# Optimization experiments

Hardware: AMD Instinct MI355X
Metric: run time of the kernel (lower is better)

The kernel has to match this reference:

```python
import jax, jax.numpy as jnp
import numpy as np

H_DIM = 1024
NUM_HEADS = 16
HEAD_DIM = H_DIM // NUM_HEADS
EPS = 1e-5


def rms_norm(x, w, eps=EPS):
    var = jnp.mean(jnp.square(x), axis=-1, keepdims=True)
    return x * jax.lax.rsqrt(var + eps) * w


def setup_inputs() -> dict:
    key = jax.random.key(0)
    ks = jax.random.split(key, 8)
    B, S = 2, 2048
    x = jax.random.normal(ks[0], (B, S, H_DIM), dtype=jnp.float32)
    # learned params (orthogonal init approximated by scaled normal for a correctness baseline)
    qkv_w = jax.random.normal(ks[1], (3 * H_DIM, H_DIM), dtype=jnp.float32) / np.sqrt(H_DIM)
    gate_w = jax.random.normal(ks[2], (NUM_HEADS, H_DIM), dtype=jnp.float32) / np.sqrt(H_DIM)
    o_w = jax.random.normal(ks[3], (H_DIM, H_DIM), dtype=jnp.float32) / np.sqrt(H_DIM)
    prenorm_w = jnp.ones((H_DIM,), dtype=jnp.float32)
    q_norm_w = jnp.ones((HEAD_DIM,), dtype=jnp.float32)
    k_norm_w = jnp.ones((HEAD_DIM,), dtype=jnp.float32)
    return {"x": x, "prenorm_w": prenorm_w, "qkv_w": qkv_w, "gate_w": gate_w,
            "o_w": o_w, "q_norm_w": q_norm_w, "k_norm_w": k_norm_w}


def reference(x, prenorm_w, qkv_w, gate_w, o_w, q_norm_w, k_norm_w):
    B, S, D = x.shape
    residual = x
    xn = rms_norm(x, prenorm_w)                                   # [B,S,D]
    qkv = jnp.einsum('bsd,ed->bse', xn, qkv_w)                    # [B,S,3D]
    qkv = qkv.reshape(B, S, 3, NUM_HEADS, HEAD_DIM)
    gate = jnp.einsum('bsd,hd->bsh', xn, gate_w)                  # [B,S,H]
    q, k, v = qkv[:, :, 0], qkv[:, :, 1], qkv[:, :, 2]            # [B,S,H,hd]
    q = rms_norm(q, q_norm_w)
    k = rms_norm(k, k_norm_w)
    scale = 1.0 / np.sqrt(HEAD_DIM).astype(np.float32)
    scores = jnp.einsum('bqhd,bkhd->bhqk', q, k) * scale          # [B,H,S,S]
    attn = jax.nn.softmax(scores, axis=-1)
    out = jnp.einsum('bhqk,bkhd->bhqd', attn, v)                  # [B,H,S,hd]
    out = out * jax.nn.sigmoid(gate).transpose(0, 2, 1)[..., None]
    out = out.transpose(0, 2, 1, 3).reshape(B, S, D)              # [B,S,D]
    return jnp.einsum('bsd,ed->bse', out, o_w) + residual
```

## Files before the change

kernel.cpp:

```cpp
#include <hip/hip_runtime.h>
#include <math.h>

typedef __bf16 bf16x8 __attribute__((ext_vector_type(8)));
typedef float f32x4 __attribute__((ext_vector_type(4)));
typedef float f32x16 __attribute__((ext_vector_type(16)));
typedef unsigned int uint2v __attribute__((ext_vector_type(2)));
typedef unsigned int uint4v __attribute__((ext_vector_type(4)));
typedef unsigned short ushort_t;

#define SEQ 2048
#define MROWS 4096
#define EPS 1e-5f
#define QKS 3200
#define LOG2E 1.4426950408889634f
#define SMAX_B2 17.32f

__device__ __forceinline__ float bf2f(ushort_t u) {
  union { unsigned int i; float f; } c; c.i = ((unsigned int)u) << 16; return c.f;
}
__device__ __forceinline__ ushort_t f2bf(float f) {
  union { unsigned int i; float f; } c; c.f = f;
  unsigned int i = c.i;
  unsigned int r = i + 0x7fffu + ((i >> 16) & 1u);
  return (ushort_t)(r >> 16);
}
__device__ __forceinline__ ushort_t f2bf_fast(float f) {
  union { __bf16 b; ushort_t u; } cv; cv.b = (__bf16)f; return cv.u;
}

__device__ __forceinline__ float exp2_raw(float x) {
  float r; asm("v_exp_f32 %0, %1" : "=v"(r) : "v"(x)); return r;
}

#define CVTPK(d, a, b) asm("v_cvt_pk_bf16_f32 %0, %1, %2" : "=v"(d) : "v"(a), "v"(b))

__device__ __forceinline__ void plane_swap(unsigned int &a, unsigned int &b) {
#if __has_builtin(__builtin_amdgcn_permlane32_swap)
  uint2v r = __builtin_amdgcn_permlane32_swap(a, b, 0, 0);
  a = r.x; b = r.y;
#else
  unsigned int sa = (unsigned int)__shfl_xor((int)a, 32);
  unsigned int sb = (unsigned int)__shfl_xor((int)b, 32);
  int hi = (int)((threadIdx.x & 63) >> 5);
  unsigned int na = hi ? sb : a;
  unsigned int nb = hi ? b : sa;
  a = na; b = nb;
#endif
}

__device__ __forceinline__ void softmax_pack(const f32x16 &stv, float &lp,
                                             uint4v &Fa, uint4v &Fb) {
  float p[16];
  #pragma unroll
  for (int r = 0; r < 16; ++r) p[r] = exp2_raw(stv[r] - SMAX_B2);
  float s0 = (p[0] + p[1]) + (p[2] + p[3]);
  float s1 = (p[4] + p[5]) + (p[6] + p[7]);
  float s2 = (p[8] + p[9]) + (p[10] + p[11]);
  float s3 = (p[12] + p[13]) + (p[14] + p[15]);
  lp += (s0 + s1) + (s2 + s3);
  unsigned int X00, X01, X10, X11, X20, X21, X30, X31;
  CVTPK(X00, p[0], p[1]);   CVTPK(X01, p[2], p[3]);
  CVTPK(X10, p[4], p[5]);   CVTPK(X11, p[6], p[7]);
  CVTPK(X20, p[8], p[9]);   CVTPK(X21, p[10], p[11]);
  CVTPK(X30, p[12], p[13]); CVTPK(X31, p[14], p[15]);
  plane_swap(X00, X10); plane_swap(X01, X11);
  plane_swap(X20, X30); plane_swap(X21, X31);
  Fa.x = X00; Fa.y = X01; Fa.z = X10; Fa.w = X11;
  Fb.x = X20; Fb.y = X21; Fb.z = X30; Fb.w = X31;
}

__device__ __forceinline__ float wave_sum(float v) {
  #pragma unroll
  for (int off = 32; off > 0; off >>= 1) v += __shfl_xor(v, off);
  return v;
}

__global__ void detect_kernel(const unsigned int* __restrict__ xraw, int* __restrict__ flag) {
  int tid = threadIdx.x;
  int cnt = 0;
  for (int i = tid; i < 4096; i += 256) {
    unsigned int e = (xraw[i] >> 7) & 0xFFu;
    cnt += (e >= 100u && e <= 150u) ? 1 : 0;
  }
  __shared__ int sred[256];
  sred[tid] = cnt;
  __syncthreads();
  for (int s = 128; s > 0; s >>= 1) {
    if (tid < s) sred[tid] += sred[tid + s];
    __syncthreads();
  }
  if (tid == 0) flag[0] = (sred[0] > 2048) ? 1 : 0;
}

__global__ void prep_norm_kernel(const void* __restrict__ qkvw_in, const void* __restrict__ gw_in,
                                 const void* __restrict__ ow_in, const void* __restrict__ pw_in,
                                 const void* __restrict__ qn_in, const void* __restrict__ kn_in,
                                 const void* __restrict__ xraw,
                                 ushort_t* __restrict__ Wcat, ushort_t* __restrict__ ow,
                                 float* __restrict__ qnf, float* __restrict__ knf,
                                 ushort_t* __restrict__ xn,
                                 const int* __restrict__ flag) {
  __shared__ float red[4];
  int bid = blockIdx.x, tid = threadIdx.x;
  int bf = *flag;
  if (bid < 3072) {
    long long i4 = (long long)bid * 256 + tid;
    if (bf) {
      ((ushort4*)Wcat)[i4] = ((const ushort4*)qkvw_in)[i4];
    } else {
      float4 f = ((const float4*)qkvw_in)[i4];
      ushort4 o;
      o.x = f2bf(f.x); o.y = f2bf(f.y); o.z = f2bf(f.z); o.w = f2bf(f.w);
      ((ushort4*)Wcat)[i4] = o;
    }
  } else if (bid < 3088) {
    long long j4 = (long long)(bid - 3072) * 256 + tid;
    ushort4* dst = (ushort4*)(Wcat + 3072 * 1024);
    if (bf) {
      dst[j4] = ((const ushort4*)gw_in)[j4];
    } else {
      float4 f = ((const float4*)gw_in)[j4];
      ushort4 o;
      o.x = f2bf(f.x); o.y = f2bf(f.y); o.z = f2bf(f.z); o.w = f2bf(f.w);
      dst[j4] = o;
    }
  } else if (bid < 4112) {
    long long j4 = (long long)(bid - 3088) * 256 + tid;
    if (bf) {
      ((ushort4*)ow)[j4] = ((const ushort4*)ow_in)[j4];
    } else {
      float4 f = ((const float4*)ow_in)[j4];
      ushort4 o;
      o.x = f2bf(f.x); o.y = f2bf(f.y); o.z = f2bf(f.z); o.w = f2bf(f.w);
      ((ushort4*)ow)[j4] = o;
    }
  } else if (bid == 4112) {
    if (tid < 64) {
      qnf[tid] = bf ? bf2f(((const ushort_t*)qn_in)[tid]) : ((const float*)qn_in)[tid];
      knf[tid] = bf ? bf2f(((const ushort_t*)kn_in)[tid]) : ((const float*)kn_in)[tid];
    }
  } else {
    int row = bid - 4113;
    float4 u;
    if (bf) {
      ushort4 s = ((const ushort4*)xraw)[row * 256 + tid];
      u.x = bf2f(s.x); u.y = bf2f(s.y); u.z = bf2f(s.z); u.w = bf2f(s.w);
    } else {
      u = ((const float4*)xraw)[row * 256 + tid];
    }
    float ss = u.x*u.x + u.y*u.y + u.z*u.z + u.w*u.w;
    ss = wave_sum(ss);
    if ((tid & 63) == 0) red[tid >> 6] = ss;
    __syncthreads();
    float total = red[0] + red[1] + red[2] + red[3];
    float inv = rsqrtf(total * (1.0f / 1024.0f) + EPS);
    float4 wu;
    if (bf) {
      ushort4 s = ((const ushort4*)pw_in)[tid];
      wu.x = bf2f(s.x); wu.y = bf2f(s.y); wu.z = bf2f(s.z); wu.w = bf2f(s.w);
    } else {
      wu = ((const float4*)pw_in)[tid];
    }
    ushort4 o;
    o.x = f2bf(u.x * inv * wu.x);
    o.y = f2bf(u.y * inv * wu.y);
    o.z = f2bf(u.z * inv * wu.z);
    o.w = f2bf(u.w * inv * wu.w);
    ((ushort4*)(xn + (long long)row * 1024))[tid] = o;
  }
}

__device__ __forceinline__ void gll16(const ushort_t* g, ushort_t* l) {
  __builtin_amdgcn_global_load_lds(
      (const __attribute__((address_space(1))) unsigned int*)g,
      (__attribute__((address_space(3))) unsigned int*)l, 16, 0, 0);
}

__global__ void gemm_qkv_fused(const ushort_t* __restrict__ A, const ushort_t* __restrict__ B,
                               ushort_t* __restrict__ C, float* __restrict__ gate,
                               ushort_t* __restrict__ Vt,
                               const float* __restrict__ qw, const float* __restrict__ kw) {
  __shared__ char gsm[128 * 136 * 2] __attribute__((aligned(16)));
  ushort_t* As = (ushort_t*)gsm;
  ushort_t* Bs = (ushort_t*)(gsm + 16384);
  int tid = threadIdx.x, wave = tid >> 6, lane = tid & 63;
  int lin = blockIdx.x;
  int xcd = lin & 7;
  int i2 = lin >> 3;
  int my = (xcd << 2) + i2 / 25;
  int nx = i2 % 25;
  int m_blk = my * 128, n_blk = nx * 128;
  int wm = (wave & 1) * 64, wn = (wave >> 1) * 64;
  int g = lane >> 4, c = lane & 15;
  int arow = lane >> 2;
  int akc = (lane & 3) << 3;
  f32x4 acc[4][4] = {};
  for (int kt = 0; kt < 1024; kt += 64) {
    #pragma unroll
    for (int hh = 0; hh < 2; ++hh)
      #pragma unroll
      for (int i = 0; i < 2; ++i) {
        int rbase = (i * 4 + wave) * 16;
        gll16(A + (long long)(m_blk + rbase + arow) * 1024 + kt + hh * 32 + akc,
              &As[hh * 4096 + rbase * 32]);
        gll16(B + (long long)(n_blk + rbase + arow) * 1024 + kt + hh * 32 + akc,
              &Bs[hh * 4096 + rbase * 32]);
      }
    __syncthreads();
    #pragma unroll
    for (int hh = 0; hh < 2; ++hh) {
      bf16x8 af[4], bfr[4];
      #pragma unroll
      for (int mi = 0; mi < 4; ++mi)
        af[mi] = *(const bf16x8*)&As[hh * 4096 + (wm + mi * 16 + c) * 32 + (g << 3)];
      #pragma unroll
      for (int ni = 0; ni < 4; ++ni)
        bfr[ni] = *(const bf16x8*)&Bs[hh * 4096 + (wn + ni * 16 + c) * 32 + (g << 3)];
      #pragma unroll
      for (int mi = 0; mi < 4; ++mi)
        #pragma unroll
        for (int ni = 0; ni < 4; ++ni)
          acc[mi][ni] = __builtin_amdgcn_mfma_f32_16x16x32_bf16(af[mi], bfr[ni], acc[mi][ni], 0, 0, 0);
    }
    __syncthreads();
  }
  int col_base = n_blk + wn;
  if (col_base < 2048) {
    int isk = col_base >= 1024;
    float scale = isk ? 1.0f : (0.125f * LOG2E);
    const float* nw = isk ? kw : qw;
    float w[4];
    #pragma unroll
    for (int ni = 0; ni < 4; ++ni) w[ni] = nw[ni * 16 + c];
    #pragma unroll
    for (int mi = 0; mi < 4; ++mi)
      #pragma unroll
      for (int r = 0; r < 4; ++r) {
        float ss = 0.f;
        #pragma unroll
        for (int ni = 0; ni < 4; ++ni) ss += acc[mi][ni][r] * acc[mi][ni][r];
        #pragma unroll
        for (int off = 8; off > 0; off >>= 1) ss += __shfl_xor(ss, off);
        float inv = rsqrtf(ss * (1.0f / 64.0f) + EPS) * scale;
        int row = m_blk + wm + mi * 16 + g * 4 + r;
        #pragma unroll
        for (int ni = 0; ni < 4; ++ni)
          C[(long long)row * QKS + col_base + ni * 16 + c] = f2bf(acc[mi][ni][r] * inv * w[ni]);
      }
  } else if (n_blk < 3072) {
    ushort_t* vts = (ushort_t*)gsm;
    const int VSTR = 136;
    #pragma unroll
    for (int mi = 0; mi < 4; ++mi)
      #pragma unroll
      for (int r = 0; r < 4; ++r) {
        int row_l = wm + mi * 16 + g * 4 + r;
        #pragma unroll
        for (int ni = 0; ni < 4; ++ni) {
          int col_l = wn + ni * 16 + c;
          vts[col_l * VSTR + row_l] = f2bf(acc[mi][ni][r]);
        }
      }
    __syncthreads();
    int rowv = tid >> 1, half = tid & 1;
    int vcol = (n_blk - 2048) + rowv;
    int h = vcol >> 6, d = vcol & 63;
    int b2 = m_blk >> 11;
    ushort_t* dst = Vt + ((long long)(b2 * 16 + h) * 64 + d) * SEQ + (m_blk & 2047) + half * 64;
    const ushort_t* srcl = &vts[rowv * VSTR + half * 64];
    #pragma unroll
    for (int j = 0; j < 8; ++j)
      *(bf16x8*)(dst + j * 8) = *(const bf16x8*)(srcl + j * 8);
  } else if (col_base == 3072) {
    #pragma unroll
    for (int mi = 0; mi < 4; ++mi)
      #pragma unroll
      for (int r = 0; r < 4; ++r) {
        int row = m_blk + wm + mi * 16 + g * 4 + r;
        float v = acc[mi][0][r];
        gate[(long long)row * 16 + c] = 1.0f / (1.0f + __expf(-v));
      }
  }
}

__global__ void gemm_tiled(const ushort_t* __restrict__ A, const ushort_t* __restrict__ B,
                           void* __restrict__ Cv, const void* __restrict__ res,
                           const int* __restrict__ flag,
                           int K, int lda, int ldb, int ldc) {
  __shared__ ushort_t As[2 * 128 * 32];
  __shared__ ushort_t Bs[2 * 128 * 32];
  int tid = threadIdx.x, wave = tid >> 6, lane = tid & 63;
  int lin = blockIdx.x;
  int xcd = lin & 7;
  int i2 = lin >> 3;
  int my = (xcd << 2) + (i2 >> 3);
  int nx = i2 & 7;
  int m_blk = my * 128, n_blk = nx * 128;
  int wm = (wave & 1) * 64, wn = (wave >> 1) * 64;
  int g = lane >> 4, c = lane & 15;
  int arow = lane >> 2;
  int akc = (lane & 3) << 3;
  f32x4 acc[4][4] = {};
  for (int kt = 0; kt < K; kt += 64) {
    #pragma unroll
    for (int hh = 0; hh < 2; ++hh)
      #pragma unroll
      for (int i = 0; i < 2; ++i) {
        int rbase = (i * 4 + wave) * 16;
        gll16(A + (long long)(m_blk + rbase + arow) * lda + kt + hh * 32 + akc,
              &As[hh * 4096 + rbase * 32]);
        gll16(B + (long long)(n_blk + rbase + arow) * ldb + kt + hh * 32 + akc,
              &Bs[hh * 4096 + rbase * 32]);
      }
    __syncthreads();
    #pragma unroll
    for (int hh = 0; hh < 2; ++hh) {
      bf16x8 af[4], bfr[4];
      #pragma unroll
      for (int mi = 0; mi < 4; ++mi)
        af[mi] = *(const bf16x8*)&As[hh * 4096 + (wm + mi * 16 + c) * 32 + (g << 3)];
      #pragma unroll
      for (int ni = 0; ni < 4; ++ni)
        bfr[ni] = *(const bf16x8*)&Bs[hh * 4096 + (wn + ni * 16 + c) * 32 + (g << 3)];
      #pragma unroll
      for (int mi = 0; mi < 4; ++mi)
        #pragma unroll
        for (int ni = 0; ni < 4; ++ni)
          acc[mi][ni] = __builtin_amdgcn_mfma_f32_16x16x32_bf16(af[mi], bfr[ni], acc[mi][ni], 0, 0, 0);
    }
    __syncthreads();
  }
  int outbf = flag ? *flag : 1;
  #pragma unroll
  for (int mi = 0; mi < 4; ++mi)
    #pragma unroll
    for (int ni = 0; ni < 4; ++ni)
      #pragma unroll
      for (int r = 0; r < 4; ++r) {
        int row = m_blk + wm + mi * 16 + g * 4 + r;
        int col = n_blk + wn + ni * 16 + c;
        long long idx = (long long)row * ldc + col;
        float v = acc[mi][ni][r];
        if (res) v += outbf ? bf2f(((const ushort_t*)res)[idx]) : ((const float*)res)[idx];
        if (outbf) ((ushort_t*)Cv)[idx] = f2bf(v);
        else       ((float*)Cv)[idx] = v;
      }
}

__global__ __launch_bounds__(256, 4)
void flash_kernel(const ushort_t* __restrict__ qkv, const ushort_t* __restrict__ Vt,
                  const float* __restrict__ gate, ushort_t* __restrict__ ao) {
  __shared__ char smem[32768] __attribute__((aligned(16)));
  ushort_t* KsB = (ushort_t*)smem;
  ushort_t* VsB = (ushort_t*)(smem + 16384);
  int tid = threadIdx.x, wave = tid >> 6, lane = tid & 63;
  int al = lane & 31, hi = lane >> 5;
  int fal = (al & 7) ^ ((al >> 3) & 3);
  int qh = wave & 1, kh = wave >> 1;
  int khb = kh * 32;
  int bid = blockIdx.x;
  int xcd = bid & 7, idx = bid >> 3;
  int bh = (xcd << 2) | (idx >> 5);
  int q0 = (idx & 31) * 64;
  int b = bh >> 4, h = bh & 15;
  const ushort_t* qbase = qkv + (long long)b * SEQ * QKS + h * 64;
  const ushort_t* kbase = qbase + 1024;
  const ushort_t* vtbase = Vt + (long long)bh * 64 * SEQ;
  int qrow = q0 + qh * 32 + al;
  bf16x8 bq0 = *(const bf16x8*)(qbase + (long long)qrow * QKS + 0 * 16 + hi * 8);
  bf16x8 bq1 = *(const bf16x8*)(qbase + (long long)qrow * QKS + 1 * 16 + hi * 8);
  bf16x8 bq2 = *(const bf16x8*)(qbase + (long long)qrow * QKS + 2 * 16 + hi * 8);
  bf16x8 bq3 = *(const bf16x8*)(qbase + (long long)qrow * QKS + 3 * 16 + hi * 8);
  asm volatile("s_waitcnt vmcnt(0)"
               :
               : "v"(__builtin_bit_cast(f32x4, bq0)), "v"(__builtin_bit_cast(f32x4, bq1)),
                 "v"(__builtin_bit_cast(f32x4, bq2)), "v"(__builtin_bit_cast(f32x4, bq3))
               : "memory");
  f32x16 oac0 = {}, oac1 = {};
  float lp = 0.f;
  int srow = lane >> 3;
  int schk = lane & 7;

  #define STAGE(BUF, S0) do {                                                        \
    int gch = ((schk ^ srow ^ wave) & 7) << 3;                                       \
    int lbo = (BUF) * 4096;                                                          \
    _Pragma("unroll")                                                                \
    for (int tt = 0; tt < 2; ++tt) {                                                 \
      int rb = tt * 32 + wave * 8;                                                   \
      int row = rb + srow;                                                           \
      gll16(kbase + (long long)((S0) + row) * QKS + gch, &KsB[lbo + rb * 64]);       \
      gll16(vtbase + (long long)row * SEQ + (S0) + gch, &VsB[lbo + rb * 64]);        \
    } } while (0)

  #define PIPE_BAR(N) do {                                                           \
    asm volatile("s_waitcnt vmcnt(" #N ")" ::: "memory");                            \
    __builtin_amdgcn_s_barrier();                                                    \
    asm volatile("" ::: "memory");                                                   \
  } while (0)

  #define COMPUTE(BUF) do {                                                          \
    int lbo = (BUF) * 4096;                                                          \
    f32x16 st = {};                                                                  \
    __builtin_amdgcn_s_setprio(1);                                                   \
    _Pragma("unroll")                                                                \
    for (int dst = 0; dst < 4; ++dst) {                                              \
      int ph = (((dst << 1) | hi) ^ fal) << 3;                                       \
      bf16x8 ak = *(const bf16x8*)&KsB[lbo + (khb + al) * 64 + ph];                  \
      bf16x8 qq = (dst == 0) ? bq0 : (dst == 1) ? bq1 : (dst == 2) ? bq2 : bq3;      \
      st = __builtin_amdgcn_mfma_f32_32x32x16_bf16(ak, qq, st, 0, 0, 0);             \
    }                                                                                \
    __builtin_amdgcn_s_setprio(0);                                                   \
    uint4v Fa, Fb;                                                                   \
    softmax_pack(st, lp, Fa, Fb);                                                    \
    bf16x8 pf0 = __builtin_bit_cast(bf16x8, Fa);                                     \
    bf16x8 pf1 = __builtin_bit_cast(bf16x8, Fb);                                     \
    __builtin_amdgcn_s_setprio(1);                                                   \
    _Pragma("unroll")                                                                \
    for (int kst = 0; kst < 2; ++kst) {                                              \
      int kg = kh * 2 + kst;                                                         \
      int ph = (((kg << 1) | hi) ^ fal) << 3;                                        \
      bf16x8 av0 = *(const bf16x8*)&VsB[lbo + al * 64 + ph];                         \
      bf16x8 av1 = *(const bf16x8*)&VsB[lbo + (32 + al) * 64 + ph];                  \
      bf16x8 pf = kst ? pf1 : pf0;                                                   \
      oac0 = __builtin_amdgcn_mfma_f32_32x32x16_bf16(av0, pf, oac0, 0, 0, 0);        \
      oac1 = __builtin_amdgcn_mfma_f32_32x32x16_bf16(av1, pf, oac1, 0, 0, 0);        \
    }                                                                                \
    __builtin_amdgcn_s_setprio(0);                                                   \
  } while (0)

  STAGE(0, 0);
  for (int it = 0; it < 31; ++it) {
    STAGE((it + 1) & 1, (it + 1) * 64);
    PIPE_BAR(4);
    COMPUTE(it & 1);
    __builtin_amdgcn_s_barrier();
  }
  PIPE_BAR(0);
  COMPUTE(1);
  #undef STAGE
  #undef PIPE_BAR
  #undef COMPUTE

  float ltot = lp + __shfl_xor(lp, 32);
  float* cbuf = (float*)smem;
  float* lbuf = cbuf + 64 * 65;
  int qrl = qh * 32 + al;
  __syncthreads();
  if (kh == 1) {
    #pragma unroll
    for (int r = 0; r < 16; ++r) {
      int d = (r & 3) + 8 * (r >> 2) + 4 * hi;
      cbuf[qrl * 65 + d]      = oac0[r];
      cbuf[qrl * 65 + 32 + d] = oac1[r];
    }
    if (hi == 0) lbuf[qrl] = ltot;
  }
  __syncthreads();
  if (kh == 0) {
    ltot += lbuf[qrl];
    #pragma unroll
    for (int r = 0; r < 16; ++r) {
      int d = (r & 3) + 8 * (r >> 2) + 4 * hi;
      oac0[r] += cbuf[qrl * 65 + d];
      oac1[r] += cbuf[qrl * 65 + 32 + d];
    }
    float sg = gate[(long long)(b * SEQ + qrow) * 16 + h];
    float scale = sg / ltot;
    ushort_t* aobase = ao + (long long)(b * SEQ + qrow) * 1024 + h * 64;
    #define OSTORE(OA, MT) do {                                                      \
      _Pragma("unroll")                                                              \
      for (int tt = 0; tt < 4; ++tt) {                                               \
        ushort4 o;                                                                   \
        o.x = f2bf_fast(OA[4 * tt + 0] * scale);                                     \
        o.y = f2bf_fast(OA[4 * tt + 1] * scale);                                     \
        o.z = f2bf_fast(OA[4 * tt + 2] * scale);                                     \
        o.w = f2bf_fast(OA[4 * tt + 3] * scale);                                     \
        *(ushort4*)(aobase + (MT) * 32 + 8 * tt + 4 * hi) = o;                       \
      } } while (0)
    OSTORE(oac0, 0);
    OSTORE(oac1, 1);
    #undef OSTORE
  }
}

extern "C" void kernel_launch(void* const* d_in, const int* in_sizes, int n_in,
                              void* d_out, int out_size, void* d_ws, size_t ws_size,
                              hipStream_t stream) {
  (void)in_sizes; (void)n_in; (void)out_size; (void)ws_size;
  char* ws = (char*)d_ws;
  ushort_t* Wcat = (ushort_t*)(ws);
  ushort_t* ow   = (ushort_t*)(ws + (7ll << 20));
  float*    qnf  = (float*)   (ws + (9ll << 20) + (8 << 10));
  float*    knf  = (float*)   (ws + (9ll << 20) + (12 << 10));
  int*      flag = (int*)     (ws + (9ll << 20) + (16 << 10));
  float*    gate = (float*)   (ws + (9ll << 20) + (64 << 10));
  ushort_t* xn   = (ushort_t*)(ws + (10ll << 20));
  ushort_t* qkv2 = (ushort_t*)(ws + (18ll << 20));
  ushort_t* Vt   = (ushort_t*)(ws + (44ll << 20));
  ushort_t* ao   = (ushort_t*)(ws + (52ll << 20));

  detect_kernel<<<1, 256, 0, stream>>>((const unsigned int*)d_in[0], flag);
  prep_norm_kernel<<<8209, 256, 0, stream>>>(d_in[2], d_in[3], d_in[4], d_in[1], d_in[5], d_in[6],
                                             d_in[0], Wcat, ow, qnf, knf, xn, flag);
  gemm_qkv_fused<<<dim3(800), 256, 0, stream>>>(xn, Wcat, qkv2, gate, Vt, qnf, knf);
  flash_kernel<<<dim3(1024), 256, 0, stream>>>(qkv2, Vt, gate, ao);
  gemm_tiled<<<dim3(256), 256, 0, stream>>>(ao, ow, d_out, d_in[0], flag,
                                            1024, 1024, 1024, 1024);
}
```

Measured before the change: 218.4 us.

## Double-buffer LDS tiles in QKV and tiled GEMMs with explicit vmcnt waits

Both GEMM kernels now prefetch the next K tile into a second LDS buffer while computing the current one. They wait with s_waitcnt vmcnt(N) plus a raw barrier instead of two __syncthreads per iteration. The QKV kernel switches to 32-wide K stages, and MFMA sections are wrapped in s_setprio to favour the matrix issue. The aim is to hide global-to-LDS load latency behind compute. The cost is doubled LDS in gemm_tiled, which may lower occupancy, and hand-counted vmcnt values that must match the number of outstanding loads.

```diff
diff --git a/kernel.cpp b/kernel.cpp
--- a/kernel.cpp
+++ b/kernel.cpp
@@ -195,35 +195,54 @@
   int arow = lane >> 2;
   int akc = (lane & 3) << 3;
   f32x4 acc[4][4] = {};
-  for (int kt = 0; kt < 1024; kt += 64) {
-    #pragma unroll
-    for (int hh = 0; hh < 2; ++hh)
-      #pragma unroll
-      for (int i = 0; i < 2; ++i) {
-        int rbase = (i * 4 + wave) * 16;
-        gll16(A + (long long)(m_blk + rbase + arow) * 1024 + kt + hh * 32 + akc,
-              &As[hh * 4096 + rbase * 32]);
-        gll16(B + (long long)(n_blk + rbase + arow) * 1024 + kt + hh * 32 + akc,
-              &Bs[hh * 4096 + rbase * 32]);
-      }
-    __syncthreads();
-    #pragma unroll
-    for (int hh = 0; hh < 2; ++hh) {
-      bf16x8 af[4], bfr[4];
-      #pragma unroll
-      for (int mi = 0; mi < 4; ++mi)
-        af[mi] = *(const bf16x8*)&As[hh * 4096 + (wm + mi * 16 + c) * 32 + (g << 3)];
-      #pragma unroll
-      for (int ni = 0; ni < 4; ++ni)
-        bfr[ni] = *(const bf16x8*)&Bs[hh * 4096 + (wn + ni * 16 + c) * 32 + (g << 3)];
-      #pragma unroll
-      for (int mi = 0; mi < 4; ++mi)
-        #pragma unroll
-        for (int ni = 0; ni < 4; ++ni)
-          acc[mi][ni] = __builtin_amdgcn_mfma_f32_16x16x32_bf16(af[mi], bfr[ni], acc[mi][ni], 0, 0, 0);
-    }
-    __syncthreads();
-  }
+
+  #define GSTAGE(BB, KT) do {                                                        \
+    int lbo = (BB) * 4096;                                                           \
+    _Pragma("unroll")                                                                \
+    for (int ii = 0; ii < 2; ++ii) {                                                 \
+      int rbase = (ii * 4 + wave) * 16;                                              \
+      gll16(A + (long long)(m_blk + rbase + arow) * 1024 + (KT) + akc, &As[lbo + rbase * 32]); \
+      gll16(B + (long long)(n_blk + rbase + arow) * 1024 + (KT) + akc, &Bs[lbo + rbase * 32]); \
+    } } while (0)
+
+  #define GBAR(N) do {                                                               \
+    asm volatile("s_waitcnt vmcnt(" #N ")" ::: "memory");                            \
+    __builtin_amdgcn_s_barrier();                                                    \
+    asm volatile("" ::: "memory");                                                   \
+  } while (0)
+
+  #define GCOMP(BB) do {                                                             \
+    int lbo = (BB) * 4096;                                                           \
+    bf16x8 af[4], bfr[4];                                                            \
+    _Pragma("unroll")                                                                \
+    for (int mi = 0; mi < 4; ++mi)                                                   \
+      af[mi] = *(const bf16x8*)&As[lbo + (wm + mi * 16 + c) * 32 + (g << 3)];        \
+    _Pragma("unroll")                                                                \
+    for (int ni = 0; ni < 4; ++ni)                                                   \
+      bfr[ni] = *(const bf16x8*)&Bs[lbo + (wn + ni * 16 + c) * 32 + (g << 3)];       \
+    __builtin_amdgcn_s_setprio(1);                                                   \
+    _Pragma("unroll")                                                                \
+    for (int mi = 0; mi < 4; ++mi)                                                   \
+      _Pragma("unroll")                                                              \
+      for (int ni = 0; ni < 4; ++ni)                                                 \
+        acc[mi][ni] = __builtin_amdgcn_mfma_f32_16x16x32_bf16(af[mi], bfr[ni], acc[mi][ni], 0, 0, 0); \
+    __builtin_amdgcn_s_setprio(0);                                                   \
+  } while (0)
+
+  GSTAGE(0, 0);
+  for (int kt2 = 0; kt2 < 31; ++kt2) {
+    GSTAGE((kt2 + 1) & 1, (kt2 + 1) * 32);
+    GBAR(4);
+    GCOMP(kt2 & 1);
+    __builtin_amdgcn_s_barrier();
+  }
+  GBAR(0);
+  GCOMP(1);
+  #undef GSTAGE
+  #undef GBAR
+  #undef GCOMP
+  __syncthreads();
+
   int col_base = n_blk + wn;
   if (col_base < 2048) {
     int isk = col_base >= 1024;
@@ -287,8 +306,8 @@
                            void* __restrict__ Cv, const void* __restrict__ res,
                            const int* __restrict__ flag,
                            int K, int lda, int ldb, int ldc) {
-  __shared__ ushort_t As[2 * 128 * 32];
-  __shared__ ushort_t Bs[2 * 128 * 32];
+  __shared__ ushort_t As[2 * 2 * 128 * 32];
+  __shared__ ushort_t Bs[2 * 2 * 128 * 32];
   int tid = threadIdx.x, wave = tid >> 6, lane = tid & 63;
   int lin = blockIdx.x;
   int xcd = lin & 7;
@@ -301,35 +320,60 @@
   int arow = lane >> 2;
   int akc = (lane & 3) << 3;
   f32x4 acc[4][4] = {};
-  for (int kt = 0; kt < K; kt += 64) {
-    #pragma unroll
-    for (int hh = 0; hh < 2; ++hh)
-      #pragma unroll
-      for (int i = 0; i < 2; ++i) {
-        int rbase = (i * 4 + wave) * 16;
-        gll16(A + (long long)(m_blk + rbase + arow) * lda + kt + hh * 32 + akc,
-              &As[hh * 4096 + rbase * 32]);
-        gll16(B + (long long)(n_blk + rbase + arow) * ldb + kt + hh * 32 + akc,
-              &Bs[hh * 4096 + rbase * 32]);
-      }
-    __syncthreads();
-    #pragma unroll
-    for (int hh = 0; hh < 2; ++hh) {
-      bf16x8 af[4], bfr[4];
-      #pragma unroll
-      for (int mi = 0; mi < 4; ++mi)
-        af[mi] = *(const bf16x8*)&As[hh * 4096 + (wm + mi * 16 + c) * 32 + (g << 3)];
-      #pragma unroll
-      for (int ni = 0; ni < 4; ++ni)
-        bfr[ni] = *(const bf16x8*)&Bs[hh * 4096 + (wn + ni * 16 + c) * 32 + (g << 3)];
-      #pragma unroll
-      for (int mi = 0; mi < 4; ++mi)
-        #pragma unroll
-        for (int ni = 0; ni < 4; ++ni)
-          acc[mi][ni] = __builtin_amdgcn_mfma_f32_16x16x32_bf16(af[mi], bfr[ni], acc[mi][ni], 0, 0, 0);
-    }
-    __syncthreads();
-  }
+
+  #define TSTAGE(BB, KT) do {                                                        \
+    int lbo = (BB) * 8192;                                                           \
+    _Pragma("unroll")                                                                \
+    for (int hh2 = 0; hh2 < 2; ++hh2)                                                \
+      _Pragma("unroll")                                                              \
+      for (int ii = 0; ii < 2; ++ii) {                                               \
+        int rbase = (ii * 4 + wave) * 16;                                            \
+        gll16(A + (long long)(m_blk + rbase + arow) * lda + (KT) + hh2 * 32 + akc,   \
+              &As[lbo + hh2 * 4096 + rbase * 32]);                                   \
+        gll16(B + (long long)(n_blk + rbase + arow) * ldb + (KT) + hh2 * 32 + akc,   \
+              &Bs[lbo + hh2 * 4096 + rbase * 32]);                                   \
+      } } while (0)
+
+  #define TBAR(N) do {                                                               \
+    asm volatile("s_waitcnt vmcnt(" #N ")" ::: "memory");                            \
+    __builtin_amdgcn_s_barrier();                                                    \
+    asm volatile("" ::: "memory");                                                   \
+  } while (0)
+
+  #define TCOMP(BB) do {                                                             \
+    int lbo = (BB) * 8192;                                                           \
+    _Pragma("unroll")                                                                \
+    for (int hh2 = 0; hh2 < 2; ++hh2) {                                              \
+      bf16x8 af[4], bfr[4];                                                          \
+      _Pragma("unroll")                                                              \
+      for (int mi = 0; mi < 4; ++mi)                                                 \
+        af[mi] = *(const bf16x8*)&As[lbo + hh2 * 4096 + (wm + mi * 16 + c) * 32 + (g << 3)]; \
+      _Pragma("unroll")                                                              \
+      for (int ni = 0; ni < 4; ++ni)                                                 \
+        bfr[ni] = *(const bf16x8*)&Bs[lbo + hh2 * 4096 + (wn + ni * 16 + c) * 32 + (g << 3)]; \
+      __builtin_amdgcn_s_setprio(1);                                                 \
+      _Pragma("unroll")                                                              \
+      for (int mi = 0; mi < 4; ++mi)                                                 \
+        _Pragma("unroll")                                                            \
+        for (int ni = 0; ni < 4; ++ni)                                               \
+          acc[mi][ni] = __builtin_amdgcn_mfma_f32_16x16x32_bf16(af[mi], bfr[ni], acc[mi][ni], 0, 0, 0); \
+      __builtin_amdgcn_s_setprio(0);                                                 \
+    } } while (0)
+
+  int ntile = K >> 6;
+  TSTAGE(0, 0);
+  for (int t2 = 0; t2 < ntile - 1; ++t2) {
+    TSTAGE((t2 + 1) & 1, (t2 + 1) * 64);
+    TBAR(8);
+    TCOMP(t2 & 1);
+    __builtin_amdgcn_s_barrier();
+  }
+  TBAR(0);
+  TCOMP((ntile - 1) & 1);
+  #undef TSTAGE
+  #undef TBAR
+  #undef TCOMP
+
   int outbf = flag ? *flag : 1;
   #pragma unroll
   for (int mi = 0; mi < 4; ++mi)
```

New measurement: 218.6 us, median of 2. About the same (+0.1%).
